# Performance work log

Measured on AMD Instinct MI355X. Metric: run time of the kernel, lower is better.

Reference implementation:

```python
import jax, jax.numpy as jnp
import numpy as np

B, N, DEG = 16, 64, 16          # batch, nodes, out-degree per node
IN_F, EDGE_F, OUT_F, H = 1024, 128, 512, 8
F = OUT_F // H                   # n_hidden = 64 (is_concat=True)
E = N * DEG                      # num_edges = 1024
SLOPE = 0.2                      # leaky relu negative slope


def setup_inputs() -> dict:
    key = jax.random.key(0)
    k0, k1, k2, k3, k4 = jax.random.split(key, 5)
    h = jax.random.normal(k0, (B, N, IN_F), dtype=jnp.float32)
    edge_attr = jax.random.normal(k1, (B, E, EDGE_F), dtype=jnp.float32)
    # deterministic adjacency: node i -> nodes (i+k) % N, k=0..DEG-1
    # (includes self-loop, so every softmax row has >=1 neighbor)
    adj = np.zeros((N, N), dtype=np.float32)
    for i in range(N):
        for k in range(DEG):
            adj[i, (i + k) % N] = 1.0
    adj_mat = jnp.asarray(np.broadcast_to(adj, (B, N, N)).copy())
    W_node = jax.random.normal(k2, (IN_F, H * F), dtype=jnp.float32) * 0.03
    W_edge = jax.random.normal(k3, (EDGE_F, H * F), dtype=jnp.float32) * 0.05
    w_attn = jax.random.normal(k4, (3 * F,), dtype=jnp.float32) * 0.1
    return {"h": h, "adj_mat": adj_mat, "edge_attr": edge_attr,
            "W_node": W_node, "W_edge": W_edge, "w_attn": w_attn}


def reference(h, adj_mat, edge_attr, W_node, W_edge, w_attn):
    # node / edge projections
    g = (h @ W_node).reshape(B, N, H, F)                  # [B,N,H,F]
    e_proj = (edge_attr @ W_edge).reshape(B, E, H, F)     # [B,E,H,F]
    # pad edge rows up to N*N (mirrors torch.cat with zero pad)
    e_proj = jnp.pad(e_proj, ((0, 0), (0, N * N - E), (0, 0), (0, 0)))
    # scatter edge features to flattened nonzero adjacency positions,
    # in row-major nonzero order == rank via exclusive cumsum
    idx = adj_mat.reshape(B, N * N).astype(jnp.int32)     # [B,N*N] of 0/1
    rank = jnp.cumsum(idx, axis=1) - idx                  # position among nonzeros
    ef = jnp.take_along_axis(e_proj, rank[:, :, None, None], axis=1)
    ef = ef * idx[:, :, None, None].astype(g.dtype)       # zero where no edge
    ef = ef.reshape(B, N, N, H, F)                        # [B,i,j,H,F]
    # attn(cat[g_i, g_j, edge]) == g_i.w1 + g_j.w2 + edge.w3
    w_i, w_j, w_e = w_attn[:F], w_attn[F:2 * F], w_attn[2 * F:]
    s_i = jnp.einsum('bnhf,f->bnh', g, w_i)
    s_j = jnp.einsum('bnhf,f->bnh', g, w_j)
    s_e = jnp.einsum('bijhf,f->bijh', ef, w_e)
    e = jax.nn.leaky_relu(s_i[:, :, None, :] + s_j[:, None, :, :] + s_e, SLOPE)
    e = jnp.where(adj_mat[..., None] > 0, e, -jnp.inf)    # mask non-edges
    a = jax.nn.softmax(e, axis=2)                         # softmax over j
    # dropout is identity in eval mode
    out = jnp.einsum('bijh,bjhf->bihf', a, g)             # weighted aggregation
    return out.reshape(B, N, H * F)                       # is_concat=True
```

## Files before the change

kernel.cpp:

```cpp
#include <hip/hip_runtime.h>
#include <hip/hip_bf16.h>
#include <stdint.h>

#define BB 16
#define NN 64
#define DEG 16
#define IN_F 1024
#define EDGE_F 128
#define OUT_FT 512
#define HH 8
#define FF 64
#define EE (NN*DEG)
#define SLOPE 0.2f

typedef short s16x8 __attribute__((ext_vector_type(8)));
typedef float f32x4 __attribute__((ext_vector_type(4)));

__device__ __forceinline__ unsigned short f2bf(float x) {
    union { float f; uint32_t u; } v; v.f = x;
    uint32_t u = v.u;
    return (unsigned short)((u + 0x7FFFu + ((u >> 16) & 1u)) >> 16);
}

__global__ __launch_bounds__(256)
void prep_kernel(const float* __restrict__ W_node,
                 const float* __restrict__ W_edge,
                 const float* __restrict__ w_attn,
                 const float* __restrict__ adj,
                 unsigned short* __restrict__ W_T,
                 float* __restrict__ wv,
                 int* __restrict__ row_start)
{
    int bx = blockIdx.x;
    int tid = threadIdx.x;

    if (bx < 128) {
        __shared__ float tile[64][65];
        int tn = bx & 7, tk = bx >> 3;
        int k0 = tk * 64, n0 = tn * 64;
        #pragma unroll
        for (int j = 0; j < 16; ++j) {
            int lin = j * 256 + tid;
            int r = lin >> 6, c = lin & 63;
            tile[r][c] = W_node[(size_t)(k0 + r) * 512 + n0 + c];
        }
        __syncthreads();
        #pragma unroll
        for (int j = 0; j < 16; ++j) {
            int lin = j * 256 + tid;
            int nr = lin >> 6, kc = lin & 63;
            W_T[(size_t)(n0 + nr) * 1024 + k0 + kc] = f2bf(tile[kc][nr]);
        }
    } else if (bx < 144) {
        int b = bx - 128;
        if (tid < 64) {
            const float* row = adj + (size_t)b * 4096 + (size_t)tid * 64;
            int cnt = 0;
            #pragma unroll 8
            for (int j = 0; j < 64; ++j) cnt += (row[j] > 0.5f) ? 1 : 0;
            int inc = cnt;
            #pragma unroll
            for (int d = 1; d < 64; d <<= 1) {
                int u = __shfl_up(inc, d, 64);
                if (tid >= d) inc += u;
            }
            row_start[b * 64 + tid] = inc - cnt;
        }
    } else {
        int c = tid & 127;
        int half = tid >> 7;
        const float* we = w_attn + 2 * FF;
        #pragma unroll
        for (int hh = 0; hh < 4; ++hh) {
            int h = half * 4 + hh;
            float s = 0.f;
            const float* row = W_edge + (size_t)c * 512 + h * 64;
            #pragma unroll 8
            for (int f = 0; f < 64; ++f) s += row[f] * we[f];
            wv[c * 8 + h] = s;
        }
    }
}

__global__ __launch_bounds__(256)
void main_kernel(const float* __restrict__ hmat,
                 const unsigned short* __restrict__ W_T,
                 const float* __restrict__ edge_attr,
                 const float* __restrict__ wv,
                 const float* __restrict__ w_attn,
                 float* __restrict__ g,
                 float* __restrict__ s_e,
                 float* __restrict__ s_i,
                 float* __restrict__ s_j)
{
    __shared__ __align__(16) unsigned short As[64][40];
    __shared__ __align__(16) unsigned short Bs[64][40];
    __shared__ float wvs[1024];

    int bx = blockIdx.x;
    int tid = threadIdx.x;

    if (bx < 128) {
        int head = bx & 7, mt = bx >> 3;
        int n0 = head * 64, m0 = mt * 64;
        int wave = tid >> 6, lane = tid & 63;
        int l15 = lane & 15, quad = lane >> 4;
        int wv16 = wave * 16;

        int ldr = tid >> 2;
        int ldc8 = (tid & 3) * 8;

        f32x4 acc[4];
        #pragma unroll
        for (int i = 0; i < 4; ++i) acc[i] = (f32x4){0.f, 0.f, 0.f, 0.f};

        for (int k0 = 0; k0 < 1024; k0 += 32) {
            const float* ap = hmat + (size_t)(m0 + ldr) * 1024 + k0 + ldc8;
            float4 a0 = *(const float4*)ap;
            float4 a1 = *(const float4*)(ap + 4);
            s16x8 av;
            av[0] = (short)f2bf(a0.x); av[1] = (short)f2bf(a0.y);
            av[2] = (short)f2bf(a0.z); av[3] = (short)f2bf(a0.w);
            av[4] = (short)f2bf(a1.x); av[5] = (short)f2bf(a1.y);
            av[6] = (short)f2bf(a1.z); av[7] = (short)f2bf(a1.w);
            *(s16x8*)&As[ldr][ldc8] = av;
            *(int4*)&Bs[ldr][ldc8] =
                *(const int4*)(W_T + (size_t)(n0 + ldr) * 1024 + k0 + ldc8);
            __syncthreads();

            s16x8 af = *(const s16x8*)&As[wv16 + l15][quad * 8];
            #pragma unroll
            for (int nt = 0; nt < 4; ++nt) {
                s16x8 bf = *(const s16x8*)&Bs[nt * 16 + l15][quad * 8];
                acc[nt] = __builtin_amdgcn_mfma_f32_16x16x32_bf16(af, bf, acc[nt], 0, 0, 0);
            }
            __syncthreads();
        }

        float wi[4], wj[4];
        #pragma unroll
        for (int nt = 0; nt < 4; ++nt) {
            wi[nt] = w_attn[nt * 16 + l15];
            wj[nt] = w_attn[64 + nt * 16 + l15];
        }
        float pi[4], pj[4];
        #pragma unroll
        for (int reg = 0; reg < 4; ++reg) { pi[reg] = 0.f; pj[reg] = 0.f; }

        #pragma unroll
        for (int nt = 0; nt < 4; ++nt) {
            #pragma unroll
            for (int reg = 0; reg < 4; ++reg) {
                int gm = m0 + wv16 + quad * 4 + reg;
                int gn = n0 + nt * 16 + l15;
                g[(size_t)gm * 512 + gn] = acc[nt][reg];
                pi[reg] += acc[nt][reg] * wi[nt];
                pj[reg] += acc[nt][reg] * wj[nt];
            }
        }
        #pragma unroll
        for (int mask = 1; mask < 16; mask <<= 1) {
            #pragma unroll
            for (int reg = 0; reg < 4; ++reg) {
                pi[reg] += __shfl_xor(pi[reg], mask);
                pj[reg] += __shfl_xor(pj[reg], mask);
            }
        }
        if (l15 == 0) {
            #pragma unroll
            for (int reg = 0; reg < 4; ++reg) {
                int r = m0 + wv16 + quad * 4 + reg;
                s_i[(size_t)r * 8 + head] = pi[reg];
                s_j[(size_t)r * 8 + head] = pj[reg];
            }
        }
    } else {
        ((float4*)wvs)[tid] = ((const float4*)wv)[tid];
        __syncthreads();
        int e = (bx - 128) * 256 + tid;
        const float4* erow = (const float4*)(edge_attr + (size_t)e * 128);
        f32x4 accl = {0.f, 0.f, 0.f, 0.f};
        f32x4 acch = {0.f, 0.f, 0.f, 0.f};
        for (int c4 = 0; c4 < 32; ++c4) {
            float4 v = erow[c4];
            #pragma unroll
            for (int u = 0; u < 4; ++u) {
                int c = c4 * 4 + u;
                f32x4 w0 = *(const f32x4*)&wvs[c * 8];
                f32x4 w1 = *(const f32x4*)&wvs[c * 8 + 4];
                float x = (u == 0) ? v.x : (u == 1) ? v.y : (u == 2) ? v.z : v.w;
                accl += x * w0;
                acch += x * w1;
            }
        }
        *(f32x4*)(s_e + (size_t)e * 8)     = accl;
        *(f32x4*)(s_e + (size_t)e * 8 + 4) = acch;
    }
}

__global__ __launch_bounds__(256)
void attn_kernel(const float* __restrict__ g,
                 const float* __restrict__ adj,
                 const float* __restrict__ s_e,
                 const float* __restrict__ s_i,
                 const float* __restrict__ s_j,
                 const int*   __restrict__ row_start,
                 float* __restrict__ out)
{
    __shared__ __align__(16) float gs[16][516];
    __shared__ float se_s[16][8];
    __shared__ float sj_s[16][8];
    __shared__ float a_s[16][8];
    __shared__ float si_s[8];
    __shared__ int nbr[16];
    __shared__ int m_nb_s;

    int bi = blockIdx.x;
    int b = bi >> 6, i = bi & 63;
    int tid = threadIdx.x;

    if (tid < 64) {
        float av = adj[(size_t)b * 4096 + (size_t)i * 64 + tid];
        unsigned long long m = __ballot(av > 0.5f);
        if (av > 0.5f) {
            int before = __popcll(m & ((1ull << tid) - 1ull));
            if (before < 16) nbr[before] = tid;
        }
        if (tid == 0) {
            int c = __popcll(m);
            m_nb_s = (c > 16) ? 16 : c;
        }
    }
    __syncthreads();

    int m_nb = m_nb_s;
    int rs = row_start[bi];

    int slot = tid >> 4, l16 = tid & 15;
    if (slot < m_nb) {
        const float4* src4 = (const float4*)(g + (size_t)(b * 64 + nbr[slot]) * 512);
        #pragma unroll
        for (int j = 0; j < 8; ++j) {
            int q = j * 16 + l16;
            *(float4*)&gs[slot][q * 4] = src4[q];
        }
    }
    if (tid < 128) {
        int k = tid >> 3, h = tid & 7;
        if (k < m_nb) {
            se_s[k][h] = s_e[(size_t)(b * 1024 + rs + k) * 8 + h];
            sj_s[k][h] = s_j[(size_t)(b * 64 + nbr[k]) * 8 + h];
        }
    } else if (tid < 136) {
        si_s[tid - 128] = s_i[(size_t)bi * 8 + (tid - 128)];
    }
    __syncthreads();

    if (tid < 128) {
        int k = tid >> 3, h = tid & 7;
        if (k < m_nb) {
            float v = si_s[h] + sj_s[k][h] + se_s[k][h];
            a_s[k][h] = (v >= 0.f) ? v : SLOPE * v;
        }
    }
    __syncthreads();

    if (tid < 8) {
        int h = tid;
        float mx = -1e30f;
        for (int k = 0; k < m_nb; ++k) mx = fmaxf(mx, a_s[k][h]);
        float ssum = 0.f;
        for (int k = 0; k < m_nb; ++k) {
            float e = __expf(a_s[k][h] - mx);
            a_s[k][h] = e;
            ssum += e;
        }
        float inv = 1.f / ssum;
        for (int k = 0; k < m_nb; ++k) a_s[k][h] *= inv;
    }
    __syncthreads();

    int c0 = tid * 2;
    int h = tid >> 5;
    float a0 = 0.f, a1 = 0.f;
    for (int k = 0; k < m_nb; ++k) {
        float ak = a_s[k][h];
        a0 += ak * gs[k][c0];
        a1 += ak * gs[k][c0 + 1];
    }
    out[(size_t)bi * 512 + c0]     = a0;
    out[(size_t)bi * 512 + c0 + 1] = a1;
}

extern "C" void kernel_launch(void* const* d_in, const int* in_sizes, int n_in,
                              void* d_out, int out_size, void* d_ws, size_t ws_size,
                              hipStream_t stream) {
    const float* h_in      = (const float*)d_in[0];
    const float* adj_mat   = (const float*)d_in[1];
    const float* edge_attr = (const float*)d_in[2];
    const float* W_node    = (const float*)d_in[3];
    const float* W_edge    = (const float*)d_in[4];
    const float* w_attn    = (const float*)d_in[5];
    float* out = (float*)d_out;

    char* ws = (char*)d_ws;
    unsigned short* W_T = (unsigned short*)(ws + 0x000000);
    float* g            = (float*)(ws + 0x100000);
    float* s_e          = (float*)(ws + 0x300000);
    float* s_i          = (float*)(ws + 0x380000);
    float* s_j          = (float*)(ws + 0x388000);
    float* wv           = (float*)(ws + 0x390000);
    int*   row_start    = (int*)  (ws + 0x391000);

    prep_kernel<<<145, 256, 0, stream>>>(W_node, W_edge, w_attn, adj_mat,
                                         W_T, wv, row_start);
    main_kernel<<<192, 256, 0, stream>>>(h_in, W_T, edge_attr, wv, w_attn,
                                         g, s_e, s_i, s_j);
    attn_kernel<<<1024, 256, 0, stream>>>(g, adj_mat, s_e, s_i, s_j,
                                          row_start, out);
}
```

Before: 107.3 us.

## Double-buffer GEMM shared tiles with register prefetch; fuse leaky-relu into softmax

The node-projection GEMM loop now uses two shared-memory buffers. The next K-slice is loaded into registers before the MFMAs on the current slice, then converted and stored to the alternate buffer afterwards. This removes one barrier per iteration and lets global-load latency overlap with compute, at the cost of doubling LDS for the tiles. The aggregation kernel also folds the leaky-relu score computation into the per-head softmax thread, which saves a barrier and a shared-memory round trip but puts that work on only 8 threads. The sc[16] array assumes m_nb never exceeds 16.

```diff
diff --git a/kernel.cpp b/kernel.cpp
--- a/kernel.cpp
+++ b/kernel.cpp
@@ -93,8 +93,8 @@
                  float* __restrict__ s_i,
                  float* __restrict__ s_j)
 {
-    __shared__ __align__(16) unsigned short As[64][40];
-    __shared__ __align__(16) unsigned short Bs[64][40];
+    __shared__ __align__(16) unsigned short As[2][64][40];
+    __shared__ __align__(16) unsigned short Bs[2][64][40];
     __shared__ float wvs[1024];
 
     int bx = blockIdx.x;
@@ -110,31 +110,51 @@
         int ldr = tid >> 2;
         int ldc8 = (tid & 3) * 8;
 
+        const float* apBase = hmat + (size_t)(m0 + ldr) * 1024 + ldc8;
+        const unsigned short* bpBase = W_T + (size_t)(n0 + ldr) * 1024 + ldc8;
+
         f32x4 acc[4];
         #pragma unroll
         for (int i = 0; i < 4; ++i) acc[i] = (f32x4){0.f, 0.f, 0.f, 0.f};
 
-        for (int k0 = 0; k0 < 1024; k0 += 32) {
-            const float* ap = hmat + (size_t)(m0 + ldr) * 1024 + k0 + ldc8;
-            float4 a0 = *(const float4*)ap;
-            float4 a1 = *(const float4*)(ap + 4);
+        float4 a0 = *(const float4*)(apBase);
+        float4 a1 = *(const float4*)(apBase + 4);
+        int4   bv = *(const int4*)(bpBase);
+        {
             s16x8 av;
             av[0] = (short)f2bf(a0.x); av[1] = (short)f2bf(a0.y);
             av[2] = (short)f2bf(a0.z); av[3] = (short)f2bf(a0.w);
             av[4] = (short)f2bf(a1.x); av[5] = (short)f2bf(a1.y);
             av[6] = (short)f2bf(a1.z); av[7] = (short)f2bf(a1.w);
-            *(s16x8*)&As[ldr][ldc8] = av;
-            *(int4*)&Bs[ldr][ldc8] =
-                *(const int4*)(W_T + (size_t)(n0 + ldr) * 1024 + k0 + ldc8);
+            *(s16x8*)&As[0][ldr][ldc8] = av;
+            *(int4*)&Bs[0][ldr][ldc8] = bv;
+        }
+
+        for (int it = 0; it < 32; ++it) {
             __syncthreads();
-
-            s16x8 af = *(const s16x8*)&As[wv16 + l15][quad * 8];
+            if (it + 1 < 32) {
+                const float* ap = apBase + (it + 1) * 32;
+                a0 = *(const float4*)ap;
+                a1 = *(const float4*)(ap + 4);
+                bv = *(const int4*)(bpBase + (it + 1) * 32);
+            }
+            int cur = it & 1;
+            s16x8 af = *(const s16x8*)&As[cur][wv16 + l15][quad * 8];
             #pragma unroll
             for (int nt = 0; nt < 4; ++nt) {
-                s16x8 bf = *(const s16x8*)&Bs[nt * 16 + l15][quad * 8];
+                s16x8 bf = *(const s16x8*)&Bs[cur][nt * 16 + l15][quad * 8];
                 acc[nt] = __builtin_amdgcn_mfma_f32_16x16x32_bf16(af, bf, acc[nt], 0, 0, 0);
             }
-            __syncthreads();
+            if (it + 1 < 32) {
+                int nxt = cur ^ 1;
+                s16x8 av;
+                av[0] = (short)f2bf(a0.x); av[1] = (short)f2bf(a0.y);
+                av[2] = (short)f2bf(a0.z); av[3] = (short)f2bf(a0.w);
+                av[4] = (short)f2bf(a1.x); av[5] = (short)f2bf(a1.y);
+                av[6] = (short)f2bf(a1.z); av[7] = (short)f2bf(a1.w);
+                *(s16x8*)&As[nxt][ldr][ldc8] = av;
+                *(int4*)&Bs[nxt][ldr][ldc8] = bv;
+            }
         }
 
         float wi[4], wj[4];
@@ -256,22 +276,20 @@
     }
     __syncthreads();
 
-    if (tid < 128) {
-        int k = tid >> 3, h = tid & 7;
-        if (k < m_nb) {
-            float v = si_s[h] + sj_s[k][h] + se_s[k][h];
-            a_s[k][h] = (v >= 0.f) ? v : SLOPE * v;
-        }
-    }
-    __syncthreads();
-
     if (tid < 8) {
         int h = tid;
+        float si = si_s[h];
+        float sc[16];
         float mx = -1e30f;
-        for (int k = 0; k < m_nb; ++k) mx = fmaxf(mx, a_s[k][h]);
+        for (int k = 0; k < m_nb; ++k) {
+            float v = si + sj_s[k][h] + se_s[k][h];
+            v = (v >= 0.f) ? v : SLOPE * v;
+            sc[k] = v;
+            mx = fmaxf(mx, v);
+        }
         float ssum = 0.f;
         for (int k = 0; k < m_nb; ++k) {
-            float e = __expf(a_s[k][h] - mx);
+            float e = __expf(sc[k] - mx);
             a_s[k][h] = e;
             ssum += e;
         }
```

Measured after the change: 102.2 us. -4.7%, faster.
